# Kernel tuning notes

Hardware: AMD Instinct MI355X
Metric: run time of the kernel (lower is better)

The kernel has to match this reference:

```python
import jax, jax.numpy as jnp
import numpy as np

B, S, D, H = 4, 2048, 1024, 16
DK = D // H
INFTY = 1000000.0
INIT_SCALE = 1.2  # RandomUniform(-1.2, 1.2) kernel initializer


def setup_inputs() -> dict:
    key = jax.random.key(0)
    ks = jax.random.split(key, 6)
    x = jax.random.normal(ks[0], (B, S, D), dtype=jnp.float32)
    mask = jax.random.randint(ks[1], (B, S), 0, 2) == 1  # bool padding mask
    WQ = jax.random.uniform(ks[2], (D, D), jnp.float32, -INIT_SCALE, INIT_SCALE)
    WK = jax.random.uniform(ks[3], (D, D), jnp.float32, -INIT_SCALE, INIT_SCALE)
    WV = jax.random.uniform(ks[4], (D, D), jnp.float32, -INIT_SCALE, INIT_SCALE)
    WO = jax.random.uniform(ks[5], (D, D), jnp.float32, -INIT_SCALE, INIT_SCALE)
    return {"x": x, "mask": mask, "WQ": WQ, "WK": WK, "WV": WV, "WO": WO}


def reference(x, mask, WQ, WK, WV, WO):
    # Faithful reproduction of the layout: reshape to (B, S, d_key, n_heads)
    # then permute, matching K.reshape/K.permute_dimensions in the original.
    q = (x @ WQ).reshape(B, S, DK, H).transpose(0, 3, 1, 2)  # (B, H, S, DK)
    k = (x @ WK).reshape(B, S, DK, H).transpose(0, 3, 2, 1)  # (B, H, DK, S)
    score = jnp.matmul(q, k) / np.sqrt(DK)                   # (B, H, S, S)
    # additive key masking: score - (~mask)[B,1,1,S] * infinity
    inv_mask = (~mask).astype(x.dtype)
    score = score - inv_mask[:, None, None, :] * INFTY
    score = jax.nn.softmax(score, axis=-1)                   # att_dropout == 0
    v = (x @ WV).reshape(B, S, DK, H).transpose(0, 3, 1, 2)  # (B, H, S, DK)
    o = jnp.matmul(score, v)                                 # (B, H, S, DK)
    o = o.transpose(0, 2, 1, 3).reshape(B, S, H * DK)
    o = o @ WO                                               # (B, S, D)
    # final query-position masking + abs, as in the original
    o = jnp.abs(o * mask.astype(x.dtype)[:, :, None])
    return o
```

## Files before the change

kernel.cpp:

```cpp
#include <hip/hip_runtime.h>
#include <hip/hip_bf16.h>
#include <cstdint>
#include <cstddef>

constexpr int Bc  = 4;
constexpr int Sc  = 2048;
constexpr int Dc  = 1024;
constexpr int Hc  = 16;
constexpr int DKc = 64;
constexpr int Mtot = Bc * Sc;
constexpr float SC2  = 0.125f * 1.4426950408889634f;
constexpr float INF2 = 1000000.0f * 1.4426950408889634f;
constexpr float SXq  = 5400.0f;
constexpr float SWq  = 27166.0f;
constexpr float INVS = 1.0f / (SXq * SWq);

typedef short bf16x8 __attribute__((ext_vector_type(8)));
typedef float f32x4  __attribute__((ext_vector_type(4)));
typedef int   i32x4  __attribute__((ext_vector_type(4)));
typedef unsigned int u32x4 __attribute__((ext_vector_type(4)));

__device__ inline unsigned short bf16_rn(float f) {
    uint32_t u = __float_as_uint(f);
    uint32_t r = (u + 0x7FFFu + ((u >> 16) & 1u)) >> 16;
    return (unsigned short)r;
}
__device__ inline uint32_t pk_bf16(float a, float b) {
    uint32_t d;
    asm("v_cvt_pk_bf16_f32 %0, %1, %2" : "=v"(d) : "v"(a), "v"(b));
    return d;
}
__device__ inline int perm64(int k) {
    return (k & ~63) | (((k & 15) << 2) | ((k >> 4) & 3));
}
__device__ inline void mfma_i8(i32x4& acc, u32x4 a, u32x4 b) {
    asm volatile("v_mfma_i32_16x16x64_i8 %0, %1, %2, %0" : "+v"(acc) : "v"(a), "v"(b));
}
__device__ inline void split_i16(int fx, char& h, char& l) {
    int lo = ((fx + 128) & 255) - 128;
    h = (char)((fx - lo) >> 8);
    l = (char)lo;
}
__device__ inline void gl_lds16(const void* g, void* l) {
    __builtin_amdgcn_global_load_lds(
        (const __attribute__((address_space(1))) unsigned int*)g,
        (__attribute__((address_space(3))) unsigned int*)l, 16, 0, 0);
}

__global__ __launch_bounds__(256) void mask_norm(const void* __restrict__ mraw,
                                                 int* __restrict__ mi,
                                                 int* __restrict__ rinv,
                                                 int* __restrict__ nbv,
                                                 int* __restrict__ npadv) {
    __shared__ int fF32, fU8, fI32;
    __shared__ int part[256];
    __shared__ int nb_sh;
    if (threadIdx.x == 0) { fF32 = 0; fU8 = 0; fI32 = 0; }
    __syncthreads();
    const unsigned char* mb = (const unsigned char*)mraw;
    int aF = 0, a1 = 0, a4 = 0;
    for (int i = threadIdx.x; i < Mtot; i += 256) {
        unsigned char v = mb[i];
        if ((i & 3) == 3 && v == 0x3F) aF = 1;
        if (v) {
            if (i & 3) a1 = 1;
            else if (i & 7) a4 = 1;
        }
    }
    if (aF) fF32 = 1;
    if (a1) fU8 = 1;
    if (a4) fI32 = 1;
    __syncthreads();
    if (fF32) {
        const float* mf = (const float*)mraw;
        for (int s = threadIdx.x; s < Mtot; s += 256) mi[s] = (mf[s] != 0.0f);
    } else if (fU8) {
        for (int s = threadIdx.x; s < Mtot; s += 256) mi[s] = (mb[s] != 0);
    } else if (fI32) {
        const int* m32 = (const int*)mraw;
        for (int s = threadIdx.x; s < Mtot; s += 256) mi[s] = (m32[s] != 0);
    } else {
        const long long* m64 = (const long long*)mraw;
        for (int s = threadIdx.x; s < Mtot; s += 256) mi[s] = (m64[s] != 0);
    }
    __syncthreads();

    for (int b = 0; b < Bc; ++b) {
        const int* mrow = mi + b * Sc;
        int loc[8], cnt = 0;
        #pragma unroll
        for (int u = 0; u < 8; ++u) {
            loc[u] = mrow[threadIdx.x * 8 + u];
            cnt += loc[u];
        }
        part[threadIdx.x] = cnt;
        __syncthreads();
        if (threadIdx.x == 0) {
            int run = 0;
            for (int i = 0; i < 256; ++i) { int c = part[i]; part[i] = run; run += c; }
            nbv[b] = run;
            npadv[b] = (run + 63) & ~63;
            nb_sh = run;
        }
        __syncthreads();
        const int nbb = nb_sh;
        int pos = part[threadIdx.x];
        #pragma unroll
        for (int u = 0; u < 8; ++u) {
            const int s = threadIdx.x * 8 + u;
            if (loc[u]) {
                rinv[b * Sc + pos] = s;
                pos++;
            } else {
                rinv[b * Sc + nbb + (s - pos)] = s;
            }
        }
        __syncthreads();
    }
}

__global__ __launch_bounds__(256) void zero_pad(const int* __restrict__ nbv,
                                                const int* __restrict__ npadv,
                                                unsigned short* __restrict__ Khi,
                                                unsigned short* __restrict__ Klo,
                                                unsigned short* __restrict__ Vt) {
    const int bh = blockIdx.x;
    const int b = bh >> 4;
    const int nb = nbv[b], np = npadv[b];
    const int t = threadIdx.x;
    const size_t kbase = (size_t)bh * Sc * DKc;
    const size_t vbase = (size_t)bh * DKc * Sc;
    const int n = (np - nb) * DKc;
    for (int i = t; i < n; i += 256) {
        const int r = nb + i / DKc, c = i % DKc;
        Khi[kbase + (size_t)r * DKc + c] = 0;
        Klo[kbase + (size_t)r * DKc + c] = 0;
        Vt[vbase + (size_t)c * Sc + perm64(r)] = 0;
    }
}

__global__ __launch_bounds__(256) void quant_x(const float* __restrict__ x,
                                               unsigned short* __restrict__ xhi,
                                               signed char* __restrict__ xh8,
                                               signed char* __restrict__ xl8) {
    const int i = (blockIdx.x * 256 + threadIdx.x) * 4;
    float4 v = *reinterpret_cast<const float4*>(x + i);
    ushort4 hb;
    hb.x = bf16_rn(v.x); hb.y = bf16_rn(v.y); hb.z = bf16_rn(v.z); hb.w = bf16_rn(v.w);
    *reinterpret_cast<ushort4*>(xhi + i) = hb;
    char4 h8, l8;
    int fx;
    fx = min(max(__float2int_rn(v.x * SXq), -32640), 32640); split_i16(fx, h8.x, l8.x);
    fx = min(max(__float2int_rn(v.y * SXq), -32640), 32640); split_i16(fx, h8.y, l8.y);
    fx = min(max(__float2int_rn(v.z * SXq), -32640), 32640); split_i16(fx, h8.z, l8.z);
    fx = min(max(__float2int_rn(v.w * SXq), -32640), 32640); split_i16(fx, h8.w, l8.w);
    *reinterpret_cast<char4*>(xh8 + i) = h8;
    *reinterpret_cast<char4*>(xl8 + i) = l8;
}

template<bool PERM>
__global__ __launch_bounds__(256) void split_wt(const float* __restrict__ W,
                                                unsigned short* __restrict__ WhT) {
    __shared__ float ls[64][68];
    const int k0 = blockIdx.y * 64, n0 = blockIdx.x * 64;
    const int t = threadIdx.x;
    #pragma unroll
    for (int l = 0; l < 4; ++l) {
        const int idx = t + l * 256;
        const int r = idx >> 4, c = (idx & 15) * 4;
        *reinterpret_cast<float4*>(&ls[r][c]) =
            *reinterpret_cast<const float4*>(W + (size_t)(k0 + r) * Dc + n0 + c);
    }
    __syncthreads();
    #pragma unroll
    for (int l = 0; l < 4; ++l) {
        const int idx = t + l * 256;
        const int on = idx >> 4, kq = (idx & 15) * 4;
        #pragma unroll
        for (int j = 0; j < 4; ++j) {
            const float v = ls[kq + j][on];
            const int k  = k0 + kq + j;
            const int kd = PERM ? perm64(k) : k;
            WhT[(size_t)(n0 + on) * Dc + kd] = bf16_rn(v);
        }
    }
}

__global__ __launch_bounds__(256) void split_wt_i8(const float* __restrict__ W,
                                                   signed char* __restrict__ Wh8,
                                                   signed char* __restrict__ Wl8) {
    __shared__ float ls[64][68];
    const int k0 = blockIdx.y * 64, n0 = blockIdx.x * 64;
    const int t = threadIdx.x;
    #pragma unroll
    for (int l = 0; l < 4; ++l) {
        const int idx = t + l * 256;
        const int r = idx >> 4, c = (idx & 15) * 4;
        *reinterpret_cast<float4*>(&ls[r][c]) =
            *reinterpret_cast<const float4*>(W + (size_t)(k0 + r) * Dc + n0 + c);
    }
    __syncthreads();
    #pragma unroll
    for (int l = 0; l < 4; ++l) {
        const int idx = t + l * 256;
        const int on = idx >> 4, kq = (idx & 15) * 4;
        char4 hv, lv;
        int fx;
        fx = __float2int_rn(ls[kq + 0][on] * SWq); split_i16(fx, hv.x, lv.x);
        fx = __float2int_rn(ls[kq + 1][on] * SWq); split_i16(fx, hv.y, lv.y);
        fx = __float2int_rn(ls[kq + 2][on] * SWq); split_i16(fx, hv.z, lv.z);
        fx = __float2int_rn(ls[kq + 3][on] * SWq); split_i16(fx, hv.w, lv.w);
        const size_t o = (size_t)(n0 + on) * Dc + k0 + kq;
        *reinterpret_cast<char4*>(Wh8 + o) = hv;
        *reinterpret_cast<char4*>(Wl8 + o) = lv;
    }
}

__global__ __launch_bounds__(256) void gemm_i8qk(
    const signed char* __restrict__ Ah8, const signed char* __restrict__ Al8,
    const signed char* __restrict__ Bh8, const signed char* __restrict__ Bl8,
    const int* __restrict__ rinv, const int* __restrict__ nbv, float scale,
    unsigned short* __restrict__ O1, unsigned short* __restrict__ O2) {
    __shared__ __align__(16) signed char Ah[128 * 64];
    __shared__ __align__(16) signed char Al[128 * 64];
    __shared__ __align__(16) signed char Bh[128 * 64];
    __shared__ __align__(16) signed char Bl[128 * 64];
    const int t = threadIdx.x;
    const int n0 = blockIdx.x * 128, m0 = blockIdx.y * 128;
    const int b = m0 >> 11, mm0 = m0 & 2047;
    const int nb = nbv[b];
    if (mm0 >= nb) return;
    const int wv = t >> 6, lane = t & 63, li = lane & 15, lg = lane >> 4;
    const int wm = (wv >> 1) * 64, wn = (wv & 1) * 64;

    size_t gAr[2];
    int rowN[2];
    #pragma unroll
    for (int c = 0; c < 2; ++c) {
        const int ci  = wv * 2 + c;
        const int row = ci * 16 + (lane >> 2);
        rowN[c] = n0 + row;
        gAr[c] = ((size_t)b * Sc + rinv[b * Sc + mm0 + row]) * Dc;
    }
    const int cq = (lane & 3) * 16;

    i32x4 a1[4][4] = {};
    i32x4 a2[4][4] = {};
    asm volatile("s_nop 7" :::);

    for (int k0 = 0; k0 < Dc; k0 += 64) {
        __syncthreads();
        #pragma unroll
        for (int c = 0; c < 2; ++c) {
            const int ci = wv * 2 + c;
            const size_t ga = gAr[c] + k0 + cq;
            const size_t gb = (size_t)rowN[c] * Dc + k0 + cq;
            gl_lds16(Ah8 + ga, &Ah[ci * 1024]);
            gl_lds16(Al8 + ga, &Al[ci * 1024]);
            gl_lds16(Bh8 + gb, &Bh[ci * 1024]);
            gl_lds16(Bl8 + gb, &Bl[ci * 1024]);
        }
        __syncthreads();

        u32x4 bhf[4], blf[4];
        #pragma unroll
        for (int ni = 0; ni < 4; ++ni) {
            bhf[ni] = *reinterpret_cast<const u32x4*>(&Bh[(wn + ni * 16 + li) * 64 + lg * 16]);
            blf[ni] = *reinterpret_cast<const u32x4*>(&Bl[(wn + ni * 16 + li) * 64 + lg * 16]);
        }
        #pragma unroll
        for (int mi = 0; mi < 4; ++mi) {
            const u32x4 ahf = *reinterpret_cast<const u32x4*>(&Ah[(wm + mi * 16 + li) * 64 + lg * 16]);
            const u32x4 alf = *reinterpret_cast<const u32x4*>(&Al[(wm + mi * 16 + li) * 64 + lg * 16]);
            #pragma unroll
            for (int ni = 0; ni < 4; ++ni) {
                mfma_i8(a1[mi][ni], ahf, bhf[ni]);
                mfma_i8(a2[mi][ni], ahf, blf[ni]);
                mfma_i8(a2[mi][ni], alf, bhf[ni]);
            }
        }
    }

    asm volatile("s_nop 7\ns_nop 7\ns_nop 7" :::);

    #pragma unroll
    for (int mi = 0; mi < 4; ++mi) {
        #pragma unroll
        for (int r = 0; r < 4; ++r) {
            const int cs = mm0 + wm + mi * 16 + lg * 4 + r;
            if (cs >= nb) continue;
            #pragma unroll
            for (int ni = 0; ni < 4; ++ni) {
                const int n = n0 + wn + ni * 16 + li;
                const int h = n & 15, dk = n >> 4;
                const float f = fmaf((float)a1[mi][ni][r], 65536.0f,
                                     (float)a2[mi][ni][r] * 256.0f) * scale;
                const size_t o = ((size_t)(b * Hc + h) * Sc + cs) * DKc + dk;
                const unsigned short hi = bf16_rn(f);
                O1[o] = hi;
                O2[o] = bf16_rn(f - __uint_as_float((uint32_t)hi << 16));
            }
        }
    }
}

template<int EPI>
__global__ __launch_bounds__(256) void gemm_bf16(
    const unsigned short* __restrict__ Ahi,
    const unsigned short* __restrict__ Bhi,
    const int* __restrict__ rinv, const int* __restrict__ nbv,
    unsigned short* __restrict__ O1,
    float* __restrict__ Of) {
    __shared__ __align__(16) unsigned short Ah[128 * 32];
    __shared__ __align__(16) unsigned short Bh[128 * 32];
    const int t = threadIdx.x;
    const int n0 = blockIdx.x * 128, m0 = blockIdx.y * 128;
    const int b = m0 >> 11, mm0 = m0 & 2047;
    const int nb = nbv[b];
    const int wv = t >> 6, lane = t & 63, li = lane & 15, lg = lane >> 4;
    const int wm = (wv >> 1) * 64, wn = (wv & 1) * 64;

    if (EPI == 1 && mm0 >= nb) return;
    if (EPI == 2 && mm0 >= nb) {
        #pragma unroll
        for (int mi = 0; mi < 4; ++mi) {
            #pragma unroll
            for (int r = 0; r < 4; ++r) {
                const int cs = mm0 + wm + mi * 16 + lg * 4 + r;
                const int gs = rinv[b * Sc + cs];
                float4 z = make_float4(0.f, 0.f, 0.f, 0.f);
                #pragma unroll
                for (int ni = 0; ni < 4; ++ni) {
                    const int n = n0 + wn + ni * 16 + li;
                    Of[((size_t)(b * Sc + gs)) * Dc + n] = 0.0f;
                }
                (void)z;
            }
        }
        return;
    }

    size_t gAr[2];
    int rowN[2];
    #pragma unroll
    for (int c = 0; c < 2; ++c) {
        const int ci  = wv * 2 + c;
        const int row = ci * 16 + (lane >> 2);
        rowN[c] = n0 + row;
        if (EPI == 1)
            gAr[c] = ((size_t)b * Sc + rinv[b * Sc + mm0 + row]) * Dc;
        else
            gAr[c] = (size_t)(m0 + row) * Dc;
    }
    const int cq = (lane & 3) * 8;

    f32x4 acc[4][4] = {};

    for (int k0 = 0; k0 < Dc; k0 += 32) {
        __syncthreads();
        #pragma unroll
        for (int c = 0; c < 2; ++c) {
            const int ci = wv * 2 + c;
            gl_lds16(Ahi + gAr[c] + k0 + cq, &Ah[ci * 512]);
            gl_lds16(Bhi + (size_t)rowN[c] * Dc + k0 + cq, &Bh[ci * 512]);
        }
        __syncthreads();

        bf16x8 bhf[4];
        #pragma unroll
        for (int ni = 0; ni < 4; ++ni)
            bhf[ni] = *reinterpret_cast<const bf16x8*>(&Bh[(wn + ni * 16 + li) * 32 + lg * 8]);
        #pragma unroll
        for (int mi = 0; mi < 4; ++mi) {
            const bf16x8 ahf = *reinterpret_cast<const bf16x8*>(&Ah[(wm + mi * 16 + li) * 32 + lg * 8]);
            #pragma unroll
            for (int ni = 0; ni < 4; ++ni)
                acc[mi][ni] = __builtin_amdgcn_mfma_f32_16x16x32_bf16(ahf, bhf[ni], acc[mi][ni], 0, 0, 0);
        }
    }

    #pragma unroll
    for (int mi = 0; mi < 4; ++mi) {
        #pragma unroll
        for (int r = 0; r < 4; ++r) {
            const int cs = mm0 + wm + mi * 16 + lg * 4 + r;
            if (EPI == 1) {
                if (cs >= nb) continue;
                #pragma unroll
                for (int ni = 0; ni < 4; ++ni) {
                    const int n = n0 + wn + ni * 16 + li;
                    const int h = n & 15, dk = n >> 4;
                    O1[((size_t)(b * Hc + h) * DKc + dk) * Sc + perm64(cs)] =
                        bf16_rn(acc[mi][ni][r]);
                }
            } else {
                const int gs = rinv[b * Sc + cs];
                const bool valid = (cs < nb);
                #pragma unroll
                for (int ni = 0; ni < 4; ++ni) {
                    const int n = n0 + wn + ni * 16 + li;
                    Of[((size_t)(b * Sc + gs)) * Dc + n] =
                        valid ? fabsf(acc[mi][ni][r]) : 0.0f;
                }
            }
        }
    }
}

__global__ __launch_bounds__(256) void attn_mfma(const unsigned short* __restrict__ Qhi,
                                                 const unsigned short* __restrict__ Qlo,
                                                 const unsigned short* __restrict__ Khi,
                                                 const unsigned short* __restrict__ Klo,
                                                 const unsigned short* __restrict__ Vtg,
                                                 const int* __restrict__ nbv,
                                                 const int* __restrict__ npadv,
                                                 unsigned short* __restrict__ att) {
    constexpr int TK = 64;
    const int id  = blockIdx.x;
    const int swz = (id & 7) * 128 + (id >> 3);
    const int qb  = swz & 15;
    const int bh  = swz >> 4;
    const int b = bh >> 4, h = bh & 15;
    const int q0 = qb * 128;
    const int nb = nbv[b];
    if (q0 >= nb) return;
    const int ntile = npadv[b] >> 6;

    __shared__ __align__(16) unsigned short PsKs[128][72];
    __shared__ __align__(16) unsigned short Vs[80][72];

    const int t    = threadIdx.x;
    const int wave = t >> 6;
    const int lane = t & 63;
    const int lg   = lane >> 4;
    const int li   = lane & 15;

    {
        const int r = 64 + (t >> 4), c4 = (t & 15) * 4;
        const unsigned short val = ((t >> 4) == 0) ? (unsigned short)0x3F80 : (unsigned short)0;
        ushort4 v; v.x = val; v.y = val; v.z = val; v.w = val;
        *reinterpret_cast<ushort4*>(&Vs[r][c4]) = v;
    }

    bf16x8 qh[2][2], ql[2][2];
    #pragma unroll
    for (int hf = 0; hf < 2; ++hf) {
        const size_t qrow = ((size_t)bh * Sc + q0 + wave * 32 + hf * 16 + li) * DKc + lg * 8;
        qh[hf][0] = *reinterpret_cast<const bf16x8*>(Qhi + qrow);
        qh[hf][1] = *reinterpret_cast<const bf16x8*>(Qhi + qrow + 32);
        ql[hf][0] = *reinterpret_cast<const bf16x8*>(Qlo + qrow);
        ql[hf][1] = *reinterpret_cast<const bf16x8*>(Qlo + qrow + 32);
    }

    const size_t kbase = (size_t)bh * Sc * DKc;
    const size_t vbase = (size_t)bh * DKc * Sc;

    f32x4 accO[2][5] = {};
    float m[2][4];
    #pragma unroll
    for (int hf = 0; hf < 2; ++hf)
        #pragma unroll
        for (int r = 0; r < 4; ++r) m[hf][r] = -1e30f;

    for (int kt = 0; kt < ntile; ++kt) {
        const int k0 = kt * TK;
        __syncthreads();
        #pragma unroll
        for (int u = 0; u < 2; ++u) {
            const int idx = t + u * 256;
            const int r = idx >> 3, cc = (idx & 7) * 8;
            *reinterpret_cast<uint4*>(&PsKs[r][cc]) =
                *reinterpret_cast<const uint4*>(Khi + kbase + (size_t)(k0 + r) * DKc + cc);
            *reinterpret_cast<uint4*>(&PsKs[64 + r][cc]) =
                *reinterpret_cast<const uint4*>(Klo + kbase + (size_t)(k0 + r) * DKc + cc);
            *reinterpret_cast<uint4*>(&Vs[r][cc]) =
                *reinterpret_cast<const uint4*>(Vtg + vbase + (size_t)r * Sc + k0 + cc);
        }
        __syncthreads();

        float sc[2][4][4];
        #pragma unroll
        for (int n = 0; n < 4; ++n) {
            const bf16x8 kh0 = *reinterpret_cast<const bf16x8*>(&PsKs[n * 16 + li][lg * 8]);
            const bf16x8 kh1 = *reinterpret_cast<const bf16x8*>(&PsKs[n * 16 + li][32 + lg * 8]);
            const bf16x8 kl0 = *reinterpret_cast<const bf16x8*>(&PsKs[64 + n * 16 + li][lg * 8]);
            const bf16x8 kl1 = *reinterpret_cast<const bf16x8*>(&PsKs[64 + n * 16 + li][32 + lg * 8]);
            const float mz = (k0 + n * 16 + li < nb) ? 0.0f : INF2;
            #pragma unroll
            for (int hf = 0; hf < 2; ++hf) {
                f32x4 a = {0, 0, 0, 0};
                a = __builtin_amdgcn_mfma_f32_16x16x32_bf16(qh[hf][0], kh0, a, 0, 0, 0);
                a = __builtin_amdgcn_mfma_f32_16x16x32_bf16(qh[hf][1], kh1, a, 0, 0, 0);
                a = __builtin_amdgcn_mfma_f32_16x16x32_bf16(qh[hf][0], kl0, a, 0, 0, 0);
                a = __builtin_amdgcn_mfma_f32_16x16x32_bf16(qh[hf][1], kl1, a, 0, 0, 0);
                a = __builtin_amdgcn_mfma_f32_16x16x32_bf16(ql[hf][0], kh0, a, 0, 0, 0);
                a = __builtin_amdgcn_mfma_f32_16x16x32_bf16(ql[hf][1], kh1, a, 0, 0, 0);
                #pragma unroll
                for (int r = 0; r < 4; ++r) sc[hf][n][r] = a[r] - mz;
            }
        }
        __syncthreads();

        float mx[2][4], rs[2][4];
        #pragma unroll
        for (int hf = 0; hf < 2; ++hf)
            #pragma unroll
            for (int r = 0; r < 4; ++r)
                mx[hf][r] = fmaxf(fmaxf(sc[hf][0][r], sc[hf][1][r]),
                                  fmaxf(sc[hf][2][r], sc[hf][3][r]));
        #pragma unroll
        for (int o = 1; o < 16; o <<= 1)
            #pragma unroll
            for (int hf = 0; hf < 2; ++hf)
                #pragma unroll
                for (int r = 0; r < 4; ++r)
                    mx[hf][r] = fmaxf(mx[hf][r], __shfl_xor(mx[hf][r], o));
        #pragma unroll
        for (int hf = 0; hf < 2; ++hf)
            #pragma unroll
            for (int r = 0; r < 4; ++r) {
                const float mn = fmaxf(m[hf][r], mx[hf][r]);
                rs[hf][r] = exp2f(m[hf][r] - mn);
                m[hf][r]  = mn;
            }
        #pragma unroll
        for (int hf = 0; hf < 2; ++hf)
            #pragma unroll
            for (int r = 0; r < 4; ++r) {
                const float p0 = exp2f(sc[hf][0][r] - m[hf][r]);
                const float p1 = exp2f(sc[hf][1][r] - m[hf][r]);
                const float p2 = exp2f(sc[hf][2][r] - m[hf][r]);
                const float p3 = exp2f(sc[hf][3][r] - m[hf][r]);
                uint2 w;
                w.x = pk_bf16(p0, p1);
                w.y = pk_bf16(p2, p3);
                *reinterpret_cast<uint2*>(&PsKs[wave * 32 + hf * 16 + lg * 4 + r][li * 4]) = w;
            }

        #pragma unroll
        for (int hf = 0; hf < 2; ++hf)
            #pragma unroll
            for (int dt = 0; dt < 5; ++dt)
                #pragma unroll
                for (int r = 0; r < 4; ++r)
                    accO[hf][dt][r] *= rs[hf][r];

        #pragma unroll
        for (int c = 0; c < 2; ++c) {
            bf16x8 pa[2];
            #pragma unroll
            for (int hf = 0; hf < 2; ++hf)
                pa[hf] = *reinterpret_cast<const bf16x8*>(&PsKs[wave * 32 + hf * 16 + li][c * 32 + lg * 8]);
            #pragma unroll
            for (int dt = 0; dt < 5; ++dt) {
                const bf16x8 vb = *reinterpret_cast<const bf16x8*>(&Vs[dt * 16 + li][c * 32 + lg * 8]);
                #pragma unroll
                for (int hf = 0; hf < 2; ++hf)
                    accO[hf][dt] = __builtin_amdgcn_mfma_f32_16x16x32_bf16(pa[hf], vb, accO[hf][dt], 0, 0, 0);
            }
        }
    }

    #pragma unroll
    for (int hf = 0; hf < 2; ++hf) {
        float inv[4];
        #pragma unroll
        for (int r = 0; r < 4; ++r) {
            const float lb = __shfl(accO[hf][4][r], lane & 0x30);
            inv[r] = 1.0f / lb;
        }
        #pragma unroll
        for (int r = 0; r < 4; ++r) {
            const int q = q0 + wave * 32 + hf * 16 + lg * 4 + r;
            uint2 w;
            w.x = pk_bf16(accO[hf][0][r] * inv[r], accO[hf][1][r] * inv[r]);
            w.y = pk_bf16(accO[hf][2][r] * inv[r], accO[hf][3][r] * inv[r]);
            *reinterpret_cast<uint2*>(att + (size_t)(b * Sc + q) * Dc + h * DKc + li * 4) = w;
        }
    }
}

extern "C" void kernel_launch(void* const* d_in, const int* in_sizes, int n_in,
                              void* d_out, int out_size, void* d_ws, size_t ws_size,
                              hipStream_t stream) {
    const float* x    = (const float*)d_in[0];
    const void*  mraw = d_in[1];
    const float* WQ   = (const float*)d_in[2];
    const float* WK   = (const float*)d_in[3];
    const float* WV   = (const float*)d_in[4];
    const float* WO   = (const float*)d_in[5];
    float* out = (float*)d_out;

    int* mi    = (int*)d_ws;
    int* rinv  = mi + Mtot;
    int* nbv   = rinv + Mtot;
    int* npadv = nbv + 4;
    const size_t SZ = (size_t)Mtot * Dc;
    const size_t WSZ = (size_t)Dc * Dc;
    char* p = (char*)d_ws + 65664;
    unsigned short* xhi = (unsigned short*)p;            p += SZ * 2;
    signed char*    xh8 = (signed char*)p;               p += SZ;
    signed char*    xl8 = (signed char*)p;               p += SZ;
    unsigned short* WVh = (unsigned short*)p;            p += WSZ * 2;
    unsigned short* WOh = (unsigned short*)p;            p += WSZ * 2;
    signed char*    WQh8 = (signed char*)p;              p += WSZ;
    signed char*    WQl8 = (signed char*)p;              p += WSZ;
    signed char*    WKh8 = (signed char*)p;              p += WSZ;
    signed char*    WKl8 = (signed char*)p;              p += WSZ;
    unsigned short* Qhi = (unsigned short*)p;            p += SZ * 2;
    unsigned short* Qlo = (unsigned short*)p;            p += SZ * 2;
    unsigned short* Khi = (unsigned short*)p;            p += SZ * 2;
    unsigned short* Klo = (unsigned short*)p;            p += SZ * 2;
    unsigned short* Vt  = (unsigned short*)p;            p += SZ * 2;
    unsigned short* att = xhi;

    mask_norm<<<1, 256, 0, stream>>>(mraw, mi, rinv, nbv, npadv);
    quant_x<<<(int)(SZ / 1024), 256, 0, stream>>>(x, xhi, xh8, xl8);
    const dim3 gW(16, 16);
    split_wt_i8<<<gW, 256, 0, stream>>>(WQ, WQh8, WQl8);
    split_wt_i8<<<gW, 256, 0, stream>>>(WK, WKh8, WKl8);
    split_wt<false><<<gW, 256, 0, stream>>>(WV, WVh);
    split_wt<true ><<<gW, 256, 0, stream>>>(WO, WOh);
    zero_pad<<<dim3(64), 256, 0, stream>>>(nbv, npadv, Khi, Klo, Vt);

    const dim3 gG(Dc / 128, Mtot / 128);
    gemm_i8qk<<<gG, 256, 0, stream>>>(xh8, xl8, WQh8, WQl8, rinv, nbv, SC2 * INVS, Qhi, Qlo);
    gemm_i8qk<<<gG, 256, 0, stream>>>(xh8, xl8, WKh8, WKl8, rinv, nbv, INVS, Khi, Klo);
    gemm_bf16<1><<<gG, 256, 0, stream>>>(xhi, WVh, rinv, nbv, Vt, nullptr);

    attn_mfma<<<dim3(1024), 256, 0, stream>>>(Qhi, Qlo, Khi, Klo, Vt, nbv, npadv, att);

    gemm_bf16<2><<<gG, 256, 0, stream>>>(att, WOh, rinv, nbv, nullptr, out);
}
```

Baseline: 309.9 us.

## Split attention key range across two thread groups per block with merge

Doubles the attention block to 512 threads and splits the key tiles between two 256-thread groups, each with its own shared-memory buffers. At the end, group 1 writes its partial output, running max and sum to shared memory, and group 0 merges them flash-decoding style before writing the result. The aim is more waves per query tile to hide latency and shorten the serial key loop. The cost is doubled shared memory, higher register pressure under the 512-thread launch bound, and an extra merge step.

```diff
diff --git a/kernel.cpp b/kernel.cpp
--- a/kernel.cpp
+++ b/kernel.cpp
@@ -328,13 +328,11 @@
             for (int r = 0; r < 4; ++r) {
                 const int cs = mm0 + wm + mi * 16 + lg * 4 + r;
                 const int gs = rinv[b * Sc + cs];
-                float4 z = make_float4(0.f, 0.f, 0.f, 0.f);
                 #pragma unroll
                 for (int ni = 0; ni < 4; ++ni) {
                     const int n = n0 + wn + ni * 16 + li;
                     Of[((size_t)(b * Sc + gs)) * Dc + n] = 0.0f;
                 }
-                (void)z;
             }
         }
         return;
@@ -407,7 +405,7 @@
     }
 }
 
-__global__ __launch_bounds__(256) void attn_mfma(const unsigned short* __restrict__ Qhi,
+__global__ __launch_bounds__(512) void attn_mfma(const unsigned short* __restrict__ Qhi,
                                                  const unsigned short* __restrict__ Qlo,
                                                  const unsigned short* __restrict__ Khi,
                                                  const unsigned short* __restrict__ Klo,
@@ -425,21 +423,27 @@
     const int nb = nbv[b];
     if (q0 >= nb) return;
     const int ntile = npadv[b] >> 6;
-
-    __shared__ __align__(16) unsigned short PsKs[128][72];
-    __shared__ __align__(16) unsigned short Vs[80][72];
+    const int nt2 = (ntile + 1) >> 1;
+
+    __shared__ __align__(16) unsigned short PsKs[2][128][72];
+    __shared__ __align__(16) unsigned short Vs[2][80][72];
 
     const int t    = threadIdx.x;
-    const int wave = t >> 6;
+    const int grp  = t >> 8;
+    const int tg   = t & 255;
+    const int wave = tg >> 6;
     const int lane = t & 63;
     const int lg   = lane >> 4;
     const int li   = lane & 15;
 
+    const int myBase = grp ? nt2 : 0;
+    const int myEnd  = grp ? ntile : nt2;
+
     {
-        const int r = 64 + (t >> 4), c4 = (t & 15) * 4;
-        const unsigned short val = ((t >> 4) == 0) ? (unsigned short)0x3F80 : (unsigned short)0;
+        const int r = 64 + (tg >> 4), c4 = (tg & 15) * 4;
+        const unsigned short val = ((tg >> 4) == 0) ? (unsigned short)0x3F80 : (unsigned short)0;
         ushort4 v; v.x = val; v.y = val; v.z = val; v.w = val;
-        *reinterpret_cast<ushort4*>(&Vs[r][c4]) = v;
+        *reinterpret_cast<ushort4*>(&Vs[grp][r][c4]) = v;
     }
 
     bf16x8 qh[2][2], ql[2][2];
@@ -462,29 +466,34 @@
         #pragma unroll
         for (int r = 0; r < 4; ++r) m[hf][r] = -1e30f;
 
-    for (int kt = 0; kt < ntile; ++kt) {
+    for (int it = 0; it < nt2; ++it) {
+        const int kt = myBase + it;
+        const bool act = (kt < myEnd);
         const int k0 = kt * TK;
         __syncthreads();
-        #pragma unroll
-        for (int u = 0; u < 2; ++u) {
-            const int idx = t + u * 256;
-            const int r = idx >> 3, cc = (idx & 7) * 8;
-            *reinterpret_cast<uint4*>(&PsKs[r][cc]) =
-                *reinterpret_cast<const uint4*>(Khi + kbase + (size_t)(k0 + r) * DKc + cc);
-            *reinterpret_cast<uint4*>(&PsKs[64 + r][cc]) =
-                *reinterpret_cast<const uint4*>(Klo + kbase + (size_t)(k0 + r) * DKc + cc);
-            *reinterpret_cast<uint4*>(&Vs[r][cc]) =
-                *reinterpret_cast<const uint4*>(Vtg + vbase + (size_t)r * Sc + k0 + cc);
-        }
-        __syncthreads();
+        if (act) {
+            #pragma unroll
+            for (int u = 0; u < 2; ++u) {
+                const int idx = tg + u * 256;
+                const int r = idx >> 3, cc = (idx & 7) * 8;
+                *reinterpret_cast<uint4*>(&PsKs[grp][r][cc]) =
+                    *reinterpret_cast<const uint4*>(Khi + kbase + (size_t)(k0 + r) * DKc + cc);
+                *reinterpret_cast<uint4*>(&PsKs[grp][64 + r][cc]) =
+                    *reinterpret_cast<const uint4*>(Klo + kbase + (size_t)(k0 + r) * DKc + cc);
+                *reinterpret_cast<uint4*>(&Vs[grp][r][cc]) =
+                    *reinterpret_cast<const uint4*>(Vtg + vbase + (size_t)r * Sc + k0 + cc);
+            }
+        }
+        __syncthreads();
+        if (!act) continue;
 
         float sc[2][4][4];
         #pragma unroll
         for (int n = 0; n < 4; ++n) {
-            const bf16x8 kh0 = *reinterpret_cast<const bf16x8*>(&PsKs[n * 16 + li][lg * 8]);
-            const bf16x8 kh1 = *reinterpret_cast<const bf16x8*>(&PsKs[n * 16 + li][32 + lg * 8]);
-            const bf16x8 kl0 = *reinterpret_cast<const bf16x8*>(&PsKs[64 + n * 16 + li][lg * 8]);
-            const bf16x8 kl1 = *reinterpret_cast<const bf16x8*>(&PsKs[64 + n * 16 + li][32 + lg * 8]);
+            const bf16x8 kh0 = *reinterpret_cast<const bf16x8*>(&PsKs[grp][n * 16 + li][lg * 8]);
+            const bf16x8 kh1 = *reinterpret_cast<const bf16x8*>(&PsKs[grp][n * 16 + li][32 + lg * 8]);
+            const bf16x8 kl0 = *reinterpret_cast<const bf16x8*>(&PsKs[grp][64 + n * 16 + li][lg * 8]);
+            const bf16x8 kl1 = *reinterpret_cast<const bf16x8*>(&PsKs[grp][64 + n * 16 + li][32 + lg * 8]);
             const float mz = (k0 + n * 16 + li < nb) ? 0.0f : INF2;
             #pragma unroll
             for (int hf = 0; hf < 2; ++hf) {
@@ -499,7 +508,6 @@
                 for (int r = 0; r < 4; ++r) sc[hf][n][r] = a[r] - mz;
             }
         }
-        __syncthreads();
 
         float mx[2][4], rs[2][4];
         #pragma unroll
@@ -534,7 +542,7 @@
                 uint2 w;
                 w.x = pk_bf16(p0, p1);
                 w.y = pk_bf16(p2, p3);
-                *reinterpret_cast<uint2*>(&PsKs[wave * 32 + hf * 16 + lg * 4 + r][li * 4]) = w;
+                *reinterpret_cast<uint2*>(&PsKs[grp][wave * 32 + hf * 16 + lg * 4 + r][li * 4]) = w;
             }
 
         #pragma unroll
@@ -550,10 +558,10 @@
             bf16x8 pa[2];
             #pragma unroll
             for (int hf = 0; hf < 2; ++hf)
-                pa[hf] = *reinterpret_cast<const bf16x8*>(&PsKs[wave * 32 + hf * 16 + li][c * 32 + lg * 8]);
+                pa[hf] = *reinterpret_cast<const bf16x8*>(&PsKs[grp][wave * 32 + hf * 16 + li][c * 32 + lg * 8]);
             #pragma unroll
             for (int dt = 0; dt < 5; ++dt) {
-                const bf16x8 vb = *reinterpret_cast<const bf16x8*>(&Vs[dt * 16 + li][c * 32 + lg * 8]);
+                const bf16x8 vb = *reinterpret_cast<const bf16x8*>(&Vs[grp][dt * 16 + li][c * 32 + lg * 8]);
                 #pragma unroll
                 for (int hf = 0; hf < 2; ++hf)
                     accO[hf][dt] = __builtin_amdgcn_mfma_f32_16x16x32_bf16(pa[hf], vb, accO[hf][dt], 0, 0, 0);
@@ -561,21 +569,49 @@
         }
     }
 
-    #pragma unroll
-    for (int hf = 0; hf < 2; ++hf) {
-        float inv[4];
-        #pragma unroll
-        for (int r = 0; r < 4; ++r) {
-            const float lb = __shfl(accO[hf][4][r], lane & 0x30);
-            inv[r] = 1.0f / lb;
-        }
-        #pragma unroll
-        for (int r = 0; r < 4; ++r) {
-            const int q = q0 + wave * 32 + hf * 16 + lg * 4 + r;
-            uint2 w;
-            w.x = pk_bf16(accO[hf][0][r] * inv[r], accO[hf][1][r] * inv[r]);
-            w.y = pk_bf16(accO[hf][2][r] * inv[r], accO[hf][3][r] * inv[r]);
-            *reinterpret_cast<uint2*>(att + (size_t)(b * Sc + q) * Dc + h * DKc + li * 4) = w;
+    __syncthreads();
+    float* pO  = (float*)&PsKs[0][0][0];
+    float* pML = pO + 128 * 64;
+
+    if (grp == 1) {
+        #pragma unroll
+        for (int hf = 0; hf < 2; ++hf) {
+            #pragma unroll
+            for (int r = 0; r < 4; ++r) {
+                const int row = wave * 32 + hf * 16 + lg * 4 + r;
+                if (li == 0) {
+                    pML[row * 2]     = m[hf][r];
+                    pML[row * 2 + 1] = accO[hf][4][r];
+                }
+                float4 o = make_float4(accO[hf][0][r], accO[hf][1][r],
+                                       accO[hf][2][r], accO[hf][3][r]);
+                *reinterpret_cast<float4*>(&pO[row * 64 + li * 4]) = o;
+            }
+        }
+    }
+    __syncthreads();
+    if (grp == 0) {
+        #pragma unroll
+        for (int hf = 0; hf < 2; ++hf) {
+            #pragma unroll
+            for (int r = 0; r < 4; ++r) {
+                const int row = wave * 32 + hf * 16 + lg * 4 + r;
+                const float m1 = pML[row * 2];
+                const float l1 = pML[row * 2 + 1];
+                const float l0 = __shfl(accO[hf][4][r], lane & 0x30);
+                const float ms = fmaxf(m[hf][r], m1);
+                const float s0 = exp2f(m[hf][r] - ms);
+                const float s1 = exp2f(m1 - ms);
+                const float inv = 1.0f / (l0 * s0 + l1 * s1);
+                const float4 o1 = *reinterpret_cast<const float4*>(&pO[row * 64 + li * 4]);
+                const int q = q0 + row;
+                uint2 w;
+                w.x = pk_bf16((accO[hf][0][r] * s0 + o1.x * s1) * inv,
+                              (accO[hf][1][r] * s0 + o1.y * s1) * inv);
+                w.y = pk_bf16((accO[hf][2][r] * s0 + o1.z * s1) * inv,
+                              (accO[hf][3][r] * s0 + o1.w * s1) * inv);
+                *reinterpret_cast<uint2*>(att + (size_t)(b * Sc + q) * Dc + h * DKc + li * 4) = w;
+            }
         }
     }
 }
@@ -628,7 +664,7 @@
     gemm_i8qk<<<gG, 256, 0, stream>>>(xh8, xl8, WKh8, WKl8, rinv, nbv, INVS, Khi, Klo);
     gemm_bf16<1><<<gG, 256, 0, stream>>>(xhi, WVh, rinv, nbv, Vt, nullptr);
 
-    attn_mfma<<<dim3(1024), 256, 0, stream>>>(Qhi, Qlo, Khi, Klo, Vt, nbv, npadv, att);
+    attn_mfma<<<dim3(1024), 512, 0, stream>>>(Qhi, Qlo, Khi, Klo, Vt, nbv, npadv, att);
 
     gemm_bf16<2><<<gG, 256, 0, stream>>>(att, WOh, rinv, nbv, nullptr, out);
 }
```

Result: no change. 305.5 us (-1.4%).
